# Kernel tuning notes

Hardware: AMD Instinct MI355X
Metric: run time of the kernel (lower is better)

The kernel has to match this reference:

```python
import jax, jax.numpy as jnp
import numpy as np

B, NP, L, C, NA = 16, 512, 20, 3, 50
RATIO = 0.8
K = int(np.ceil(RATIO * NP))  # 410 nodes kept per graph
N = B * NP
E = 6 * N
NF, EF = 13, 4
EPS = 1e-5


def _graph_norm(x, w, b, ms):
    # PyG GraphNorm called WITHOUT batch in the source -> single global graph
    mean = x.mean(0)
    out = x - ms * mean
    var = (out * out).mean(0)
    return w * out / jnp.sqrt(var + EPS) + b


def _forward(x, pan_w, lin1_w, lin1_b, norm1_w, norm1_b, norm1_ms,
             pool_p, pool_beta, gat_wl, gat_bl, gat_wr, gat_br, gat_att, gat_bias,
             norm2_w, norm2_b, norm2_ms,
             val1_w, val1_b, val2_w, val2_b, val3_w, val3_b,
             adv1_w, adv1_b, adv2_w, adv2_b, adv3_w, adv3_b,
             edge_index, current_node_ids, action_mask):
    src, dst = edge_index[0], edge_index[1]
    # PANConv builds SparseTensor(row=edge_index[1], col=edge_index[0]) -> row = target
    A = jnp.zeros((B, NP, NP), x.dtype).at[dst // NP, dst % NP, src % NP].set(1.0)
    eyeB = jnp.broadcast_to(jnp.eye(NP, dtype=x.dtype), A.shape)

    # panentropy: M = sum_{i=0..L} w_i * A^i  (dense per graph)
    def step(carry, wi):
        tmp, acc = carry
        tmp = tmp @ A
        return (tmp, acc + wi * tmp), None
    (_, M), _ = jax.lax.scan(step, (eyeB, pan_w[0] * eyeB), pan_w[1:])
    deg = M.sum(-1)                                   # row sums
    dis = jnp.where(deg > 0, 1.0 / jnp.sqrt(deg), 0.0)
    Mn = dis[:, :, None] * M * dis[:, None, :]        # D^-1/2 M D^-1/2

    # conv1: propagate (Mn @ x) then Linear
    x3 = x.reshape(B, NP, NF)
    h = jnp.einsum('bij,bjf->bif', Mn, x3) @ lin1_w + lin1_b   # [B,NP,C]
    x1 = jax.nn.relu(_graph_norm(h.reshape(N, C), norm1_w, norm1_b, norm1_ms))  # [N,C]
    h = x1.reshape(B, NP, C)

    # PANPooling: score = tanh(b0 * <x,p> + b1 * colsum(Mn)); keep top K per graph
    score = jnp.tanh(pool_beta[0] * (h * pool_p).sum(-1) + pool_beta[1] * Mn.sum(-2))
    vals, idx = jax.lax.top_k(score, K)                        # [B,K]
    xp = jnp.take_along_axis(h, idx[:, :, None], axis=1) * vals[..., None]
    Mg = jax.vmap(lambda m, i: m[i][:, i])(Mn, idx)            # filtered adjacency [B,K,K]
    mask = (jnp.swapaxes(Mg, 1, 2) != 0) | jnp.eye(K, dtype=bool)  # mask[b,i,j]: edge j->i (+self loops)

    # GATv2Conv, heads=1, eval mode (no dropout), edge_attr not passed in source
    xl = xp @ gat_wl + gat_bl
    xr = xp @ gat_wr + gat_br
    e = jax.nn.leaky_relu(xr[:, :, None, :] + xl[:, None, :, :], 0.2)  # [B,i,j,C]
    logits = jnp.where(mask, jnp.einsum('bijc,c->bij', e, gat_att), -1e9)
    alpha = jax.nn.softmax(logits, axis=-1)
    g = jnp.einsum('bij,bjc->bic', alpha, xl) + gat_bias

    g = jax.nn.relu(_graph_norm(g.reshape(B * K, C), norm2_w, norm2_b, norm2_ms)).reshape(B, K, C)
    gp = g.sum(1)                                              # global_add_pool [B,C]

    # source uses POOLED bincount cumsum offsets to index the pre-pool arrays (faithful)
    gidx = current_node_ids + jnp.arange(B, dtype=current_node_ids.dtype) * K
    feat = jnp.concatenate([x[gidx], x1[gidx], gp], axis=1)    # [B,19]

    a = jax.nn.relu(feat @ adv1_w + adv1_b)
    a = jax.nn.relu(a @ adv2_w + adv2_b)
    a = a @ adv3_w + adv3_b
    v = jax.nn.relu(feat @ val1_w + val1_b)
    v = jax.nn.relu(v @ val2_w + val2_b)
    v = v @ val3_w + val3_b
    q = v + (a - a.mean(1, keepdims=True))
    return jnp.where(action_mask == 0, -1e8, q)


def setup_inputs() -> dict:
    key = jax.random.key(0)
    ks = list(jax.random.split(key, 40))
    nk = lambda: ks.pop()
    # within-graph random edges so the PyG-style batch structure is valid
    g = jax.random.randint(nk(), (E,), 0, B)
    u = jax.random.randint(nk(), (E,), 0, NP)
    v = jax.random.randint(nk(), (E,), 0, NP)
    edge_index = jnp.stack([g * NP + u, g * NP + v]).astype(jnp.int32)

    def lin(k, i, o):
        k1, k2 = jax.random.split(k)
        return (jax.random.normal(k1, (i, o), jnp.float32) / np.sqrt(i),
                jax.random.normal(k2, (o,), jnp.float32) * 0.01)

    lin1_w, lin1_b = lin(nk(), NF, C)
    gat_wl, gat_bl = lin(nk(), C, C)
    gat_wr, gat_br = lin(nk(), C, C)
    val1_w, val1_b = lin(nk(), 19, 10)
    val2_w, val2_b = lin(nk(), 10, 5)
    val3_w, val3_b = lin(nk(), 5, 1)
    adv1_w, adv1_b = lin(nk(), 19, 10)
    adv2_w, adv2_b = lin(nk(), 10, 5)
    adv3_w, adv3_b = lin(nk(), 5, NA)
    return dict(
        x=jax.random.normal(nk(), (N, NF), jnp.float32),
        edge_index=edge_index,
        edge_attr=jax.random.normal(nk(), (E, EF), jnp.float32),
        batch=jnp.arange(N, dtype=jnp.int32) // NP,
        current_node_ids=jax.random.randint(nk(), (B,), 0, NP),
        action_mask=jax.random.randint(nk(), (B, NA), 0, 2),
        pan_w=jax.random.uniform(nk(), (L + 1,), jnp.float32) * 0.5,
        lin1_w=lin1_w, lin1_b=lin1_b,
        norm1_w=jnp.ones(C), norm1_b=jnp.zeros(C), norm1_ms=jnp.ones(C),
        pool_p=jax.random.normal(nk(), (C,), jnp.float32),
        pool_beta=jnp.array([0.5, 0.5], jnp.float32),
        gat_wl=gat_wl, gat_bl=gat_bl, gat_wr=gat_wr, gat_br=gat_br,
        gat_att=jax.random.normal(nk(), (C,), jnp.float32),
        gat_bias=jax.random.normal(nk(), (C,), jnp.float32) * 0.01,
        norm2_w=jnp.ones(C), norm2_b=jnp.zeros(C), norm2_ms=jnp.ones(C),
        val1_w=val1_w, val1_b=val1_b, val2_w=val2_w, val2_b=val2_b,
        val3_w=val3_w, val3_b=val3_b,
        adv1_w=adv1_w, adv1_b=adv1_b, adv2_w=adv2_w, adv2_b=adv2_b,
        adv3_w=adv3_w, adv3_b=adv3_b,
    )


def reference(x, edge_index, edge_attr, batch, current_node_ids, action_mask,
              pan_w, lin1_w, lin1_b, norm1_w, norm1_b, norm1_ms,
              pool_p, pool_beta, gat_wl, gat_bl, gat_wr, gat_br, gat_att, gat_bias,
              norm2_w, norm2_b, norm2_ms,
              val1_w, val1_b, val2_w, val2_b, val3_w, val3_b,
              adv1_w, adv1_b, adv2_w, adv2_b, adv3_w, adv3_b):
    del edge_attr, batch  # received by the torch forward but never consumed
    return _forward(x, pan_w, lin1_w, lin1_b, norm1_w, norm1_b, norm1_ms,
                    pool_p, pool_beta, gat_wl, gat_bl, gat_wr, gat_br, gat_att, gat_bias,
                    norm2_w, norm2_b, norm2_ms,
                    val1_w, val1_b, val2_w, val2_b, val3_w, val3_b,
                    adv1_w, adv1_b, adv2_w, adv2_b, adv3_w, adv3_b,
                    edge_index, current_node_ids, action_mask)
```

## Files before the change

kernel.cpp:

```cpp
#include <hip/hip_runtime.h>
#include <hip/hip_bf16.h>
#include <stdint.h>
#include <math.h>

#define BB   16
#define NPn  512
#define LLp  20
#define NAa  50
#define KKk  410
#define NNt  (BB * NPn)
#define EEe  (6 * NNt)
#define NFf  13
#define KPAD 416
#define KP2  448
#define EPSf 1e-5f
#define QCLMP 1e6f
#define MAXD 28
#define PADR 512

__device__ __forceinline__ float r17_sane(float v) {
    if (!(v == v)) return 0.0f;
    return fminf(fmaxf(v, -1e15f), 1e15f);
}

__device__ __forceinline__ int r19_wmaxdeg(const int (&iF)[MAXD]) {
    int deg = 0;
#pragma unroll
    for (int j = 0; j < MAXD; ++j) deg += (iF[j] != PADR) ? 1 : 0;
#pragma unroll
    for (int off = 32; off; off >>= 1) {
        const int o = __shfl_xor(deg, off);
        deg = o > deg ? o : deg;
    }
    return deg;
}

__device__ __forceinline__ float r19_gsum(const float* __restrict__ rp,
                                          const int (&iF)[MAXD], int dm) {
    float s = 0.0f;
    s += rp[iF[0]]; s += rp[iF[1]]; s += rp[iF[2]]; s += rp[iF[3]];
    if (dm > 4) {
        s += rp[iF[4]]; s += rp[iF[5]]; s += rp[iF[6]]; s += rp[iF[7]];
        if (dm > 8) {
            s += rp[iF[8]]; s += rp[iF[9]]; s += rp[iF[10]]; s += rp[iF[11]];
            if (dm > 12) {
                s += rp[iF[12]]; s += rp[iF[13]]; s += rp[iF[14]]; s += rp[iF[15]];
                if (dm > 16) {
                    s += rp[iF[16]]; s += rp[iF[17]]; s += rp[iF[18]]; s += rp[iF[19]];
                    if (dm > 20) {
                        s += rp[iF[20]]; s += rp[iF[21]]; s += rp[iF[22]]; s += rp[iF[23]];
                        if (dm > 24) {
                            s += rp[iF[24]]; s += rp[iF[25]]; s += rp[iF[26]]; s += rp[iF[27]];
                        }
                    }
                }
            }
        }
    }
    return s;
}

__device__ __forceinline__ void r19_gor(const uint2* __restrict__ rp,
                                        const int (&iF)[MAXD], int dm, uint2& r) {
    {
        const uint2 v0 = rp[iF[0]], v1 = rp[iF[1]], v2 = rp[iF[2]], v3 = rp[iF[3]];
        r.x |= v0.x | v1.x | v2.x | v3.x;
        r.y |= v0.y | v1.y | v2.y | v3.y;
    }
    if (dm > 4) {
        const uint2 v0 = rp[iF[4]], v1 = rp[iF[5]], v2 = rp[iF[6]], v3 = rp[iF[7]];
        r.x |= v0.x | v1.x | v2.x | v3.x;
        r.y |= v0.y | v1.y | v2.y | v3.y;
        if (dm > 8) {
            const uint2 w0 = rp[iF[8]], w1 = rp[iF[9]], w2 = rp[iF[10]], w3 = rp[iF[11]];
            r.x |= w0.x | w1.x | w2.x | w3.x;
            r.y |= w0.y | w1.y | w2.y | w3.y;
            if (dm > 12) {
                const uint2 u0 = rp[iF[12]], u1 = rp[iF[13]], u2 = rp[iF[14]], u3 = rp[iF[15]];
                r.x |= u0.x | u1.x | u2.x | u3.x;
                r.y |= u0.y | u1.y | u2.y | u3.y;
                if (dm > 16) {
                    const uint2 a0 = rp[iF[16]], a1 = rp[iF[17]], a2 = rp[iF[18]], a3 = rp[iF[19]];
                    r.x |= a0.x | a1.x | a2.x | a3.x;
                    r.y |= a0.y | a1.y | a2.y | a3.y;
                    if (dm > 20) {
                        const uint2 b0 = rp[iF[20]], b1 = rp[iF[21]], b2 = rp[iF[22]], b3 = rp[iF[23]];
                        r.x |= b0.x | b1.x | b2.x | b3.x;
                        r.y |= b0.y | b1.y | b2.y | b3.y;
                        if (dm > 24) {
                            const uint2 c0 = rp[iF[24]], c1 = rp[iF[25]], c2 = rp[iF[26]], c3 = rp[iF[27]];
                            r.x |= c0.x | c1.x | c2.x | c3.x;
                            r.y |= c0.y | c1.y | c2.y | c3.y;
                        }
                    }
                }
            }
        }
    }
}

__global__ __launch_bounds__(256) void r17_scatter(
    const int* __restrict__ ei,
    uint32_t* __restrict__ fwdb, uint32_t* __restrict__ trsb)
{
    const int e = blockIdx.x * 256 + threadIdx.x;
    if (e < EEe) {
        const int src = ei[e], dst = ei[EEe + e];
        atomicOr(&fwdb[(size_t)dst * 16 + ((src & 511) >> 5)], 1u << (src & 31));
        atomicOr(&trsb[(size_t)src * 16 + ((dst & 511) >> 5)], 1u << (dst & 31));
    }
}

__global__ __launch_bounds__(256) void r17_extract(
    const uint32_t* __restrict__ fwdb, const uint32_t* __restrict__ trsb,
    unsigned short* __restrict__ csrF, unsigned short* __restrict__ csrT)
{
    const int t = blockIdx.x * 256 + threadIdx.x;
    const int node = t & 8191;
    const uint32_t* bs = (t < 8192) ? (fwdb + (size_t)node * 16)
                                    : (trsb + (size_t)node * 16);
    unsigned short* cs = (t < 8192) ? csrF : csrT;
    int cnt = 0;
    for (int w = 0; w < 16; ++w) {
        uint32_t bits = bs[w];
        while (bits) {
            const int u = (w << 5) + __ffs(bits) - 1;
            bits &= bits - 1;
            if (cnt < MAXD) cs[(size_t)cnt * 8192 + node] = (unsigned short)u;
            ++cnt;
        }
    }
    for (int j = cnt; j < MAXD; ++j) cs[(size_t)j * 8192 + node] = PADR;
}

__global__ __launch_bounds__(512) void r19_mid(
    const float* __restrict__ x,
    const unsigned short* __restrict__ csrF,
    const unsigned short* __restrict__ csrT,
    const float* __restrict__ panw,
    const float* __restrict__ l1w, const float* __restrict__ l1b,
    float* __restrict__ h_raw, float* __restrict__ colsum,
    uint32_t* __restrict__ Rb)
{
    __shared__ __align__(16) uint32_t sbuf[2052];
    const int b = blockIdx.x, y = blockIdx.y, t = threadIdx.x;
    const int node = b * 512 + t;

    int iF[MAXD];
#pragma unroll
    for (int j = 0; j < MAXD; ++j) iF[j] = (int)csrF[(size_t)j * 8192 + node];
    const int dmF = r19_wmaxdeg(iF);

    if (y < 4) {
        const int c = y;
        float* pa  = (float*)sbuf;
        float* pb  = (float*)(sbuf + 513);
        float* wsh = (float*)(sbuf + 1026);
        if (t < 21) wsh[t] = panw[t];

        pa[t] = 1.0f;
        if (t == 0) { pa[512] = 0.0f; pb[512] = 0.0f; }
        __syncthreads();
        float dacc = wsh[0];
        {
            float* rp = pa; float* rn = pb;
            for (int i = 1; i <= LLp; ++i) {
                const float s = r19_gsum(rp, iF, dmF);
                rn[t] = s;
                dacc += wsh[i] * s;
                __syncthreads();
                float* tp = rp; rp = rn; rn = tp;
            }
        }
        const float d0 = (dacc > 0.0f) ? 1.0f / sqrtf(dacc) : 0.0f;

        int idx[MAXD];
        int dm2;
        if (c == 3) {
#pragma unroll
            for (int j = 0; j < MAXD; ++j) idx[j] = (int)csrT[(size_t)j * 8192 + node];
            dm2 = r19_wmaxdeg(idx);
        } else {
#pragma unroll
            for (int j = 0; j < MAXD; ++j) idx[j] = iF[j];
            dm2 = dmF;
        }
        float seed;
        if (c < 3) {
            float xw = 0.0f;
            const float* xr = x + (size_t)node * NFf;
            for (int f = 0; f < NFf; ++f) xw += xr[f] * l1w[f * 3 + c];
            seed = d0 * xw;
        } else {
            seed = d0;
        }
        pa[t] = seed;
        if (t == 0) { pa[512] = 0.0f; pb[512] = 0.0f; }
        __syncthreads();
        float acc = wsh[0] * seed;
        {
            float* rp = pa; float* rn = pb;
            for (int i = 1; i <= LLp; ++i) {
                const float s = r19_gsum(rp, idx, dm2);
                rn[t] = s;
                acc += wsh[i] * s;
                __syncthreads();
                float* tp = rp; rp = rn; rn = tp;
            }
        }
        if (c < 3) h_raw[(size_t)node * 3 + c] = r17_sane(d0 * acc + l1b[c]);
        else       colsum[node] = r17_sane(d0 * acc);
    } else {
        const int q = y - 4;
        uint2* R1 = (uint2*)sbuf;
        uint2* R2 = R1 + 513;
        uint2 seed;
        seed.x = ((t >> 5) == 2 * q)     ? (1u << (t & 31)) : 0u;
        seed.y = ((t >> 5) == 2 * q + 1) ? (1u << (t & 31)) : 0u;
        R1[t] = seed;
        if (t == 0) {
            uint2 z; z.x = 0u; z.y = 0u;
            R1[512] = z; R2[512] = z;
        }
        __syncthreads();
        uint2* Rp = R1; uint2* Rn = R2;
        for (int i = 0; i < LLp; ++i) {
            uint2 r = Rp[t];
            r19_gor(Rp, iF, dmF, r);
            Rn[t] = r;
            __syncthreads();
            uint2* tp = Rp; Rp = Rn; Rn = tp;
        }
        *(uint2*)(&Rb[(size_t)node * 16 + 2 * q]) = Rp[t];
    }
}

__global__ __launch_bounds__(512) void r19_pool(
    const float* __restrict__ h_raw,
    const float* __restrict__ colsum,
    const uint32_t* __restrict__ Rb,
    const float* n1w, const float* n1b, const float* n1ms,
    const float* poolp, const float* poolb,
    const float* gwl, const float* gbl,
    float* __restrict__ x1,
    float* __restrict__ xpg,
    float4* __restrict__ xlg,
    int*   __restrict__ kidxg,
    uint32_t* __restrict__ RTg)
{
    __shared__ __align__(16) uint32_t pg[2208];
    float* sc   = (float*)pg;
    float* mv   = (float*)(pg + 512);
    float* wred = (float*)(pg + 520);
    float* xpS  = (float*)(pg + 544);
    int*   kidx = (int*)(pg + 1792);
    const int b = blockIdx.x, t = threadIdx.x;
    const int lane = t & 63, wv = t >> 6;
    const float inv_n = 1.0f / (float)NNt;

    float hv0[16], hv1[16], hv2[16];
    float p0 = 0.0f, p1 = 0.0f, p2 = 0.0f;
#pragma unroll
    for (int k = 0; k < 16; ++k) {
        const float* hr = h_raw + (size_t)(k * 512 + t) * 3;
        hv0[k] = hr[0]; hv1[k] = hr[1]; hv2[k] = hr[2];
        p0 += hv0[k]; p1 += hv1[k]; p2 += hv2[k];
    }
#pragma unroll
    for (int off = 32; off; off >>= 1) {
        p0 += __shfl_xor(p0, off); p1 += __shfl_xor(p1, off); p2 += __shfl_xor(p2, off);
    }
    if (lane == 0) { wred[wv * 3 + 0] = p0; wred[wv * 3 + 1] = p1; wred[wv * 3 + 2] = p2; }
    __syncthreads();
    if (t < 3) {
        float s = 0.0f;
        for (int w = 0; w < 8; ++w) s += wred[w * 3 + t];
        mv[t] = s * inv_n;
    }
    __syncthreads();
    const float mm0 = n1ms[0] * mv[0], mm1 = n1ms[1] * mv[1], mm2 = n1ms[2] * mv[2];
    float q0 = 0.0f, q1 = 0.0f, q2 = 0.0f;
#pragma unroll
    for (int k = 0; k < 16; ++k) {
        const float d0 = hv0[k] - mm0, d1 = hv1[k] - mm1, d2 = hv2[k] - mm2;
        q0 += d0 * d0; q1 += d1 * d1; q2 += d2 * d2;
    }
#pragma unroll
    for (int off = 32; off; off >>= 1) {
        q0 += __shfl_xor(q0, off); q1 += __shfl_xor(q1, off); q2 += __shfl_xor(q2, off);
    }
    if (lane == 0) { wred[wv * 3 + 0] = q0; wred[wv * 3 + 1] = q1; wred[wv * 3 + 2] = q2; }
    __syncthreads();
    if (t < 3) {
        float s = 0.0f;
        for (int w = 0; w < 8; ++w) s += wred[w * 3 + t];
        mv[3 + t] = s * inv_n;
    }
    __syncthreads();

    const float mmv[3] = { mm0, mm1, mm2 };
    float xv[3];
#pragma unroll
    for (int c = 0; c < 3; ++c) {
        const float iv = 1.0f / sqrtf(fmaxf(mv[3 + c], 0.0f) + EPSf);
        const float o  = h_raw[(size_t)(b * NPn + t) * 3 + c] - mmv[c];
        const float tt = n1w[c] * o * iv + n1b[c];
        xv[c] = fmaxf(tt, 0.0f);
        x1[(size_t)(b * NPn + t) * 3 + c] = xv[c];
    }
    float s = poolb[0] * (xv[0] * poolp[0] + xv[1] * poolp[1] + xv[2] * poolp[2])
            + poolb[1] * colsum[b * NPn + t];
    s = tanhf(s);
    if (!(s == s)) s = 0.0f;
    sc[t] = s;
    __syncthreads();

    int cnt = 0;
    for (int u = 0; u < NPn; u += 4) {
        const float4 s4 = *(const float4*)(sc + u);
        cnt += ((s4.x > s) || (s4.x == s && (u + 0) < t)) ? 1 : 0;
        cnt += ((s4.y > s) || (s4.y == s && (u + 1) < t)) ? 1 : 0;
        cnt += ((s4.z > s) || (s4.z == s && (u + 2) < t)) ? 1 : 0;
        cnt += ((s4.w > s) || (s4.w == s && (u + 3) < t)) ? 1 : 0;
    }
    if (cnt < KKk) {
        const float xp0 = xv[0] * s, xp1 = xv[1] * s, xp2 = xv[2] * s;
        kidx[cnt] = t;
        xpS[cnt * 3 + 0] = xp0;
        xpS[cnt * 3 + 1] = xp1;
        xpS[cnt * 3 + 2] = xp2;
        kidxg[b * KPAD + cnt] = t;
        xpg[(size_t)(b * KPAD + cnt) * 3 + 0] = xp0;
        xpg[(size_t)(b * KPAD + cnt) * 3 + 1] = xp1;
        xpg[(size_t)(b * KPAD + cnt) * 3 + 2] = xp2;
    }
    __syncthreads();

    float Wl[9];
#pragma unroll
    for (int i2 = 0; i2 < 9; ++i2) Wl[i2] = gwl[i2];
    const float Bl0 = gbl[0], Bl1 = gbl[1], Bl2 = gbl[2];
    if (t < KP2) {
        float xl0, xl1, xl2;
        uint32_t* RT = RTg + (size_t)b * 16 * KP2 + t;
        if (t < KKk) {
            const float c0 = xpS[t * 3 + 0];
            const float c1 = xpS[t * 3 + 1];
            const float c2 = xpS[t * 3 + 2];
            xl0 = c0 * Wl[0] + c1 * Wl[3] + c2 * Wl[6] + Bl0;
            xl1 = c0 * Wl[1] + c1 * Wl[4] + c2 * Wl[7] + Bl1;
            xl2 = c0 * Wl[2] + c1 * Wl[5] + c2 * Wl[8] + Bl2;
            const uint4* rr = (const uint4*)(Rb + (size_t)(b * NPn + kidx[t]) * 16);
            const uint4 r0 = rr[0], r1 = rr[1], r2 = rr[2], r3 = rr[3];
            RT[ 0 * KP2] = r0.x; RT[ 1 * KP2] = r0.y; RT[ 2 * KP2] = r0.z; RT[ 3 * KP2] = r0.w;
            RT[ 4 * KP2] = r1.x; RT[ 5 * KP2] = r1.y; RT[ 6 * KP2] = r1.z; RT[ 7 * KP2] = r1.w;
            RT[ 8 * KP2] = r2.x; RT[ 9 * KP2] = r2.y; RT[10 * KP2] = r2.z; RT[11 * KP2] = r2.w;
            RT[12 * KP2] = r3.x; RT[13 * KP2] = r3.y; RT[14 * KP2] = r3.z; RT[15 * KP2] = r3.w;
        } else {
            xl0 = 0.0f; xl1 = 0.0f; xl2 = 0.0f;
#pragma unroll
            for (int w = 0; w < 16; ++w) RT[w * KP2] = 0u;
        }
        xlg[(size_t)(b * KP2 + t)] = make_float4(xl0, xl1, xl2, 0.0f);
    }
}

__global__ __launch_bounds__(512) void r19_gat(
    const float* __restrict__ xpg,
    const float4* __restrict__ xlg,
    const int* __restrict__ kidxg,
    const uint32_t* __restrict__ RTg,
    const float* __restrict__ gwr, const float* __restrict__ gbr,
    const float* __restrict__ gatt, const float* __restrict__ gbias,
    float* __restrict__ g_raw)
{
    const int b = blockIdx.x, y = blockIdx.y, t = threadIdx.x;
    const int lane = t & 63, wv = t >> 6;
    const int i = y * 8 + wv;
    if (i >= KKk) return;

    float Wr[9];
#pragma unroll
    for (int k = 0; k < 9; ++k) Wr[k] = gwr[k];
    const float Br0 = gbr[0], Br1 = gbr[1], Br2 = gbr[2];
    const float At0 = gatt[0], At1 = gatt[1], At2 = gatt[2];
    const float Gb0 = gbias[0], Gb1 = gbias[1], Gb2 = gbias[2];

    const int bi = kidxg[b * KPAD + i];
    const float c0 = xpg[(size_t)(b * KPAD + i) * 3 + 0];
    const float c1 = xpg[(size_t)(b * KPAD + i) * 3 + 1];
    const float c2 = xpg[(size_t)(b * KPAD + i) * 3 + 2];
    const float xr0 = c0 * Wr[0] + c1 * Wr[3] + c2 * Wr[6] + Br0;
    const float xr1 = c0 * Wr[1] + c1 * Wr[4] + c2 * Wr[7] + Br1;
    const float xr2 = c0 * Wr[2] + c1 * Wr[5] + c2 * Wr[8] + Br2;

    const uint32_t mbit = 1u << (bi & 31);
    const uint32_t* Rw = RTg + (size_t)(b * 16 + (bi >> 5)) * KP2;
    const float4* xlb = xlg + (size_t)b * KP2;

    float mx = -3e38f, lsum = 0.0f, b0 = 0.0f, b1 = 0.0f, b2 = 0.0f;
#pragma unroll
    for (int it = 0; it < 7; ++it) {
        const int j = lane + it * 64;
        const uint32_t rw = Rw[j];
        const float4 xlv = xlb[j];
        const float xl0 = xlv.x, xl1 = xlv.y, xl2 = xlv.z;
        const bool valid = (rw & mbit) || (j == i);
        float e0 = xr0 + xl0; e0 = e0 > 0.0f ? e0 : 0.2f * e0;
        float e1 = xr1 + xl1; e1 = e1 > 0.0f ? e1 : 0.2f * e1;
        float e2 = xr2 + xl2; e2 = e2 > 0.0f ? e2 : 0.2f * e2;
        const float sv = At0 * e0 + At1 * e1 + At2 * e2;
        if (valid) {
            if (sv > mx) {
                const float r = __expf(mx - sv);
                lsum *= r; b0 *= r; b1 *= r; b2 *= r;
                mx = sv;
            }
            const float pj = __expf(sv - mx);
            lsum += pj;
            b0 += pj * xl0; b1 += pj * xl1; b2 += pj * xl2;
        }
    }
#pragma unroll
    for (int off = 32; off; off >>= 1) {
        const float mo = __shfl_xor(mx, off);
        const float lo = __shfl_xor(lsum, off);
        const float d0 = __shfl_xor(b0, off);
        const float d1 = __shfl_xor(b1, off);
        const float d2 = __shfl_xor(b2, off);
        const float M  = fmaxf(mx, mo);
        const float ea = __expf(mx - M), eb = __expf(mo - M);
        lsum = lsum * ea + lo * eb;
        b0 = b0 * ea + d0 * eb;
        b1 = b1 * ea + d1 * eb;
        b2 = b2 * ea + d2 * eb;
        mx = M;
    }
    if (lane == 0) {
        const float rl = 1.0f / fmaxf(lsum, 1e-30f);
        g_raw[(size_t)(b * KPAD + i) * 3 + 0] = r17_sane(b0 * rl + Gb0);
        g_raw[(size_t)(b * KPAD + i) * 3 + 1] = r17_sane(b1 * rl + Gb1);
        g_raw[(size_t)(b * KPAD + i) * 3 + 2] = r17_sane(b2 * rl + Gb2);
    }
}

__global__ __launch_bounds__(512) void r17_head(
    const float* __restrict__ g_raw,
    const float* __restrict__ x1,
    const float* __restrict__ x,
    const int* __restrict__ cnid,
    const int* __restrict__ amask,
    const float* n2w, const float* n2b, const float* n2ms,
    const float* v1w, const float* v1b,
    const float* v2w, const float* v2b,
    const float* v3w, const float* v3b,
    const float* a1w, const float* a1b,
    const float* a2w, const float* a2b,
    const float* a3w, const float* a3b,
    float* __restrict__ out)
{
    __shared__ float wred[24];
    __shared__ float mv[6];
    __shared__ float gp[3];
    __shared__ float feat[19];
    __shared__ float h1a[10], h1v[10], h2a[5], h2v[5];
    __shared__ float a3[50];
    __shared__ float vout_s, amean_s;
    const int b = blockIdx.x, t = threadIdx.x;
    const int lane = t & 63, wv = t >> 6;
    const float denom = 1.0f / (float)(BB * KKk);

    float gv0[13], gv1[13], gv2[13];
    float p0 = 0.0f, p1 = 0.0f, p2 = 0.0f;
#pragma unroll
    for (int k = 0; k < 13; ++k) {
        const int r = k * 512 + t;
        float q0 = 0.0f, q1 = 0.0f, q2 = 0.0f;
        if (r < BB * KKk) {
            const int bq = r / KKk, iq = r - bq * KKk;
            const float* gr = g_raw + (size_t)(bq * KPAD + iq) * 3;
            q0 = gr[0]; q1 = gr[1]; q2 = gr[2];
        }
        gv0[k] = q0; gv1[k] = q1; gv2[k] = q2;
        p0 += q0; p1 += q1; p2 += q2;
    }
#pragma unroll
    for (int off = 32; off; off >>= 1) {
        p0 += __shfl_xor(p0, off); p1 += __shfl_xor(p1, off); p2 += __shfl_xor(p2, off);
    }
    if (lane == 0) { wred[wv * 3 + 0] = p0; wred[wv * 3 + 1] = p1; wred[wv * 3 + 2] = p2; }
    __syncthreads();
    if (t < 3) {
        float s = 0.0f;
        for (int w = 0; w < 8; ++w) s += wred[w * 3 + t];
        mv[t] = s * denom;
    }
    __syncthreads();
    const float mm0 = n2ms[0] * mv[0], mm1 = n2ms[1] * mv[1], mm2 = n2ms[2] * mv[2];
    float q0a = 0.0f, q1a = 0.0f, q2a = 0.0f;
#pragma unroll
    for (int k = 0; k < 13; ++k) {
        const int r = k * 512 + t;
        if (r < BB * KKk) {
            const float d0 = gv0[k] - mm0, d1 = gv1[k] - mm1, d2 = gv2[k] - mm2;
            q0a += d0 * d0; q1a += d1 * d1; q2a += d2 * d2;
        }
    }
#pragma unroll
    for (int off = 32; off; off >>= 1) {
        q0a += __shfl_xor(q0a, off); q1a += __shfl_xor(q1a, off); q2a += __shfl_xor(q2a, off);
    }
    if (lane == 0) { wred[wv * 3 + 0] = q0a; wred[wv * 3 + 1] = q1a; wred[wv * 3 + 2] = q2a; }
    __syncthreads();
    if (t < 3) {
        float s = 0.0f;
        for (int w = 0; w < 8; ++w) s += wred[w * 3 + t];
        mv[3 + t] = s * denom;
    }
    __syncthreads();

    const float mmv[3] = { mm0, mm1, mm2 };
    float s3[3] = { 0.0f, 0.0f, 0.0f };
    if (t < KKk) {
        const size_t r = (size_t)(b * KPAD + t) * 3;
#pragma unroll
        for (int c = 0; c < 3; ++c) {
            const float iv = 1.0f / sqrtf(fmaxf(mv[3 + c], 0.0f) + EPSf);
            s3[c] = fmaxf((g_raw[r + c] - mmv[c]) * iv * n2w[c] + n2b[c], 0.0f);
        }
    }
    float g0 = s3[0], g1 = s3[1], g2 = s3[2];
#pragma unroll
    for (int off = 32; off; off >>= 1) {
        g0 += __shfl_xor(g0, off); g1 += __shfl_xor(g1, off); g2 += __shfl_xor(g2, off);
    }
    if (lane == 0) { wred[wv * 3 + 0] = g0; wred[wv * 3 + 1] = g1; wred[wv * 3 + 2] = g2; }
    __syncthreads();
    if (t < 3) {
        float s = 0.0f;
        for (int w = 0; w < 8; ++w) s += wred[w * 3 + t];
        gp[t] = s;
    }
    __syncthreads();

    if (t < 19) {
        const int gidx = cnid[b] + b * KKk;
        float fv;
        if (t < 13)      fv = x[(size_t)gidx * NFf + t];
        else if (t < 16) fv = x1[(size_t)gidx * 3 + (t - 13)];
        else             fv = gp[t - 16];
        feat[t] = fv;
    }
    __syncthreads();

    if (t < 10) {
        float s = a1b[t];
        for (int f = 0; f < 19; ++f) s += feat[f] * a1w[f * 10 + t];
        h1a[t] = fmaxf(s, 0.0f);
    } else if (t >= 64 && t < 74) {
        const int j = t - 64;
        float s = v1b[j];
        for (int f = 0; f < 19; ++f) s += feat[f] * v1w[f * 10 + j];
        h1v[j] = fmaxf(s, 0.0f);
    }
    __syncthreads();
    if (t < 5) {
        float s = a2b[t];
        for (int k = 0; k < 10; ++k) s += h1a[k] * a2w[k * 5 + t];
        h2a[t] = fmaxf(s, 0.0f);
    } else if (t >= 64 && t < 69) {
        const int j = t - 64;
        float s = v2b[j];
        for (int k = 0; k < 10; ++k) s += h1v[k] * v2w[k * 5 + j];
        h2v[j] = fmaxf(s, 0.0f);
    }
    __syncthreads();
    if (t < 50) {
        float s = a3b[t];
        for (int k = 0; k < 5; ++k) s += h2a[k] * a3w[k * 50 + t];
        a3[t] = s;
    } else if (t == 64) {
        float s = v3b[0];
        for (int k = 0; k < 5; ++k) s += h2v[k] * v3w[k];
        vout_s = s;
    }
    __syncthreads();
    if (t == 0) {
        float s = 0.0f;
        for (int k = 0; k < 50; ++k) s += a3[k];
        amean_s = s * (1.0f / 50.0f);
    }
    __syncthreads();
    if (t < 50) {
        float q = vout_s + a3[t] - amean_s;
        if (!(q == q)) q = 0.0f;
        q = fminf(fmaxf(q, -QCLMP), QCLMP);
        out[b * NAa + t] = (amask[b * NAa + t] == 0) ? -1e8f : q;
    }
}

extern "C" void kernel_launch(void* const* d_in, const int* in_sizes, int n_in,
                              void* d_out, int out_size, void* d_ws, size_t ws_size,
                              hipStream_t stream) {
    (void)in_sizes; (void)n_in; (void)out_size;
    const float* x     = (const float*)d_in[0];
    const int* ei      = (const int*)d_in[1];
    const int* cnid    = (const int*)d_in[4];
    const int* amask   = (const int*)d_in[5];
    const float* panw  = (const float*)d_in[6];
    const float* l1w   = (const float*)d_in[7];
    const float* l1b   = (const float*)d_in[8];
    const float* n1w   = (const float*)d_in[9];
    const float* n1b   = (const float*)d_in[10];
    const float* n1ms  = (const float*)d_in[11];
    const float* poolp = (const float*)d_in[12];
    const float* poolb = (const float*)d_in[13];
    const float* gwl   = (const float*)d_in[14];
    const float* gbl   = (const float*)d_in[15];
    const float* gwr   = (const float*)d_in[16];
    const float* gbr   = (const float*)d_in[17];
    const float* gatt  = (const float*)d_in[18];
    const float* gbias = (const float*)d_in[19];
    const float* n2w   = (const float*)d_in[20];
    const float* n2b   = (const float*)d_in[21];
    const float* n2ms  = (const float*)d_in[22];
    const float* v1w   = (const float*)d_in[23];
    const float* v1b   = (const float*)d_in[24];
    const float* v2w   = (const float*)d_in[25];
    const float* v2b   = (const float*)d_in[26];
    const float* v3w   = (const float*)d_in[27];
    const float* v3b   = (const float*)d_in[28];
    const float* a1w   = (const float*)d_in[29];
    const float* a1b   = (const float*)d_in[30];
    const float* a2w   = (const float*)d_in[31];
    const float* a2b   = (const float*)d_in[32];
    const float* a3w   = (const float*)d_in[33];
    const float* a3b   = (const float*)d_in[34];
    float* out         = (float*)d_out;

    uint8_t* wsb = (uint8_t*)d_ws;
    uint32_t* fwdb = (uint32_t*)wsb;
    uint32_t* trsb = (uint32_t*)(wsb + 524288);
    uint32_t* Rb   = (uint32_t*)(wsb + 1048576);
    unsigned short* csrF = (unsigned short*)(wsb + 1572864);
    unsigned short* csrT = csrF + (size_t)MAXD * 8192;
    float* h_raw  = (float*)(csrT + (size_t)MAXD * 8192);
    float* x1     = h_raw + (size_t)NNt * 3;
    float* colsum = x1 + (size_t)NNt * 3;
    float* g_raw  = colsum + NNt;
    float* xpg    = g_raw + (size_t)BB * KPAD * 3;
    float4* xlg   = (float4*)(xpg + (size_t)BB * KPAD * 3);
    int*   kidxg  = (int*)(xlg + (size_t)BB * KP2);
    uint32_t* RTg = (uint32_t*)(kidxg + (size_t)BB * KPAD);
    const size_t needed = 1572864
                        + 2 * (size_t)MAXD * 8192 * 2
                        + ((size_t)(2 * NNt * 3 + NNt
                           + 2 * BB * KPAD * 3)) * 4
                        + (size_t)BB * KP2 * 16
                        + (size_t)BB * KPAD * 4
                        + (size_t)BB * 16 * KP2 * 4;
    if (ws_size < needed) return;

    hipMemsetAsync(fwdb, 0, 1048576, stream);
    r17_scatter<<<dim3((EEe + 255) / 256), dim3(256), 0, stream>>>(ei, fwdb, trsb);
    r17_extract<<<dim3(64), dim3(256), 0, stream>>>(fwdb, trsb, csrF, csrT);
    r19_mid<<<dim3(16, 12), dim3(512), 0, stream>>>(x, csrF, csrT, panw, l1w, l1b,
                                                    h_raw, colsum, Rb);
    r19_pool<<<dim3(16), dim3(512), 0, stream>>>(h_raw, colsum, Rb,
                                                 n1w, n1b, n1ms, poolp, poolb,
                                                 gwl, gbl,
                                                 x1, xpg, xlg, kidxg, RTg);
    r19_gat<<<dim3(16, 52), dim3(512), 0, stream>>>(xpg, xlg, kidxg, RTg,
                                                    gwr, gbr, gatt, gbias, g_raw);
    r17_head<<<dim3(16), dim3(512), 0, stream>>>(g_raw, x1, x, cnid, amask,
                                                 n2w, n2b, n2ms, v1w, v1b, v2w, v2b, v3w, v3b,
                                                 a1w, a1b, a2w, a2b, a3w, a3b, out);
}
```

Baseline: 201.6 us.

## Fuse all stages into one persistent kernel with software grid barriers

Replaces the memset plus six separate kernel launches with a single 192-block persistent kernel. Stages are separated by atomic-counter grid barriers, and only a small barrier memset remains. The aim is to remove per-launch overhead and the inter-kernel gaps in a latency-bound pipeline. The trade-offs are spin-wait barrier cost, the assumption that all 192 blocks are co-resident, and reduced parallelism in stages that previously used more blocks (for example the GAT stage's 16x52 grid).

```diff
diff --git a/kernel.cpp b/kernel.cpp
--- a/kernel.cpp
+++ b/kernel.cpp
@@ -1,5 +1,4 @@
 #include <hip/hip_runtime.h>
-#include <hip/hip_bf16.h>
 #include <stdint.h>
 #include <math.h>
 
@@ -17,10 +16,26 @@
 #define QCLMP 1e6f
 #define MAXD 28
 #define PADR 512
+#define NBLK 192
+#define NWAVE (NBLK * 8)
 
 __device__ __forceinline__ float r17_sane(float v) {
     if (!(v == v)) return 0.0f;
     return fminf(fmaxf(v, -1e15f), 1e15f);
+}
+
+__device__ __forceinline__ void r20_gridbar(uint32_t* bar) {
+    __syncthreads();
+    if (threadIdx.x == 0) {
+        __threadfence();
+        __hip_atomic_fetch_add(bar, 1u, __ATOMIC_ACQ_REL, __HIP_MEMORY_SCOPE_AGENT);
+        while (__hip_atomic_load(bar, __ATOMIC_ACQUIRE, __HIP_MEMORY_SCOPE_AGENT)
+               < (uint32_t)NBLK) {
+            __builtin_amdgcn_s_sleep(2);
+        }
+        __threadfence();
+    }
+    __syncthreads();
 }
 
 __device__ __forceinline__ int r19_wmaxdeg(const int (&iF)[MAXD]) {
@@ -99,503 +114,486 @@
     }
 }
 
-__global__ __launch_bounds__(256) void r17_scatter(
-    const int* __restrict__ ei,
-    uint32_t* __restrict__ fwdb, uint32_t* __restrict__ trsb)
+struct R20P {
+    const float* x; const int* ei; const int* cnid; const int* amask;
+    const float* panw; const float* l1w; const float* l1b;
+    const float* n1w; const float* n1b; const float* n1ms;
+    const float* poolp; const float* poolb;
+    const float* gwl; const float* gbl; const float* gwr; const float* gbr;
+    const float* gatt; const float* gbias;
+    const float* n2w; const float* n2b; const float* n2ms;
+    const float* v1w; const float* v1b; const float* v2w; const float* v2b;
+    const float* v3w; const float* v3b;
+    const float* a1w; const float* a1b; const float* a2w; const float* a2b;
+    const float* a3w; const float* a3b;
+    uint32_t* fwdb; uint32_t* trsb; uint32_t* bar; uint32_t* Rb;
+    unsigned short* csrF; unsigned short* csrT;
+    float* h_raw; float* x1; float* colsum; float* g_raw;
+    float* xpg; float4* xlg; int* kidxg; uint32_t* RTg;
+    float* out;
+};
+
+__global__ __launch_bounds__(512) void r20_mega(R20P p)
 {
-    const int e = blockIdx.x * 256 + threadIdx.x;
-    if (e < EEe) {
-        const int src = ei[e], dst = ei[EEe + e];
-        atomicOr(&fwdb[(size_t)dst * 16 + ((src & 511) >> 5)], 1u << (src & 31));
-        atomicOr(&trsb[(size_t)src * 16 + ((dst & 511) >> 5)], 1u << (dst & 31));
-    }
-}
-
-__global__ __launch_bounds__(256) void r17_extract(
-    const uint32_t* __restrict__ fwdb, const uint32_t* __restrict__ trsb,
-    unsigned short* __restrict__ csrF, unsigned short* __restrict__ csrT)
-{
-    const int t = blockIdx.x * 256 + threadIdx.x;
-    const int node = t & 8191;
-    const uint32_t* bs = (t < 8192) ? (fwdb + (size_t)node * 16)
-                                    : (trsb + (size_t)node * 16);
-    unsigned short* cs = (t < 8192) ? csrF : csrT;
-    int cnt = 0;
-    for (int w = 0; w < 16; ++w) {
-        uint32_t bits = bs[w];
-        while (bits) {
-            const int u = (w << 5) + __ffs(bits) - 1;
-            bits &= bits - 1;
-            if (cnt < MAXD) cs[(size_t)cnt * 8192 + node] = (unsigned short)u;
-            ++cnt;
-        }
-    }
-    for (int j = cnt; j < MAXD; ++j) cs[(size_t)j * 8192 + node] = PADR;
-}
-
-__global__ __launch_bounds__(512) void r19_mid(
-    const float* __restrict__ x,
-    const unsigned short* __restrict__ csrF,
-    const unsigned short* __restrict__ csrT,
-    const float* __restrict__ panw,
-    const float* __restrict__ l1w, const float* __restrict__ l1b,
-    float* __restrict__ h_raw, float* __restrict__ colsum,
-    uint32_t* __restrict__ Rb)
-{
-    __shared__ __align__(16) uint32_t sbuf[2052];
-    const int b = blockIdx.x, y = blockIdx.y, t = threadIdx.x;
-    const int node = b * 512 + t;
-
-    int iF[MAXD];
-#pragma unroll
-    for (int j = 0; j < MAXD; ++j) iF[j] = (int)csrF[(size_t)j * 8192 + node];
-    const int dmF = r19_wmaxdeg(iF);
-
-    if (y < 4) {
-        const int c = y;
-        float* pa  = (float*)sbuf;
-        float* pb  = (float*)(sbuf + 513);
-        float* wsh = (float*)(sbuf + 1026);
-        if (t < 21) wsh[t] = panw[t];
-
-        pa[t] = 1.0f;
-        if (t == 0) { pa[512] = 0.0f; pb[512] = 0.0f; }
-        __syncthreads();
-        float dacc = wsh[0];
-        {
-            float* rp = pa; float* rn = pb;
-            for (int i = 1; i <= LLp; ++i) {
-                const float s = r19_gsum(rp, iF, dmF);
-                rn[t] = s;
-                dacc += wsh[i] * s;
+    __shared__ __align__(16) uint32_t sbuf[2208];
+    const int blk = blockIdx.x, t = threadIdx.x;
+    const int gtid = blk * 512 + t;
+    const int lane = t & 63, wv = t >> 6;
+
+    if (gtid < 65536) ((uint4*)p.fwdb)[gtid] = make_uint4(0u, 0u, 0u, 0u);
+    r20_gridbar(p.bar + 0);
+
+    if (gtid < EEe) {
+        const int src = p.ei[gtid], dst = p.ei[EEe + gtid];
+        atomicOr(&p.fwdb[(size_t)dst * 16 + ((src & 511) >> 5)], 1u << (src & 31));
+        atomicOr(&p.trsb[(size_t)src * 16 + ((dst & 511) >> 5)], 1u << (dst & 31));
+    }
+    r20_gridbar(p.bar + 1);
+
+    if (gtid < 16384) {
+        const int node = gtid & 8191;
+        const uint32_t* bs = (gtid < 8192) ? (p.fwdb + (size_t)node * 16)
+                                           : (p.trsb + (size_t)node * 16);
+        unsigned short* cs = (gtid < 8192) ? p.csrF : p.csrT;
+        int cnt = 0;
+        for (int w = 0; w < 16; ++w) {
+            uint32_t bits = bs[w];
+            while (bits) {
+                const int u = (w << 5) + __ffs(bits) - 1;
+                bits &= bits - 1;
+                if (cnt < MAXD) cs[(size_t)cnt * 8192 + node] = (unsigned short)u;
+                ++cnt;
+            }
+        }
+        for (int j = cnt; j < MAXD; ++j) cs[(size_t)j * 8192 + node] = PADR;
+    }
+    r20_gridbar(p.bar + 2);
+
+    {
+        const int b = blk / 12, y = blk % 12;
+        const int node = b * 512 + t;
+        int iF[MAXD];
+#pragma unroll
+        for (int j = 0; j < MAXD; ++j) iF[j] = (int)p.csrF[(size_t)j * 8192 + node];
+        const int dmF = r19_wmaxdeg(iF);
+
+        if (y < 4) {
+            const int c = y;
+            float* pa  = (float*)sbuf;
+            float* pb  = (float*)(sbuf + 513);
+            float* wsh = (float*)(sbuf + 1026);
+            if (t < 21) wsh[t] = p.panw[t];
+
+            pa[t] = 1.0f;
+            if (t == 0) { pa[512] = 0.0f; pb[512] = 0.0f; }
+            __syncthreads();
+            float dacc = wsh[0];
+            {
+                float* rp = pa; float* rn = pb;
+                for (int i = 1; i <= LLp; ++i) {
+                    const float s = r19_gsum(rp, iF, dmF);
+                    rn[t] = s;
+                    dacc += wsh[i] * s;
+                    __syncthreads();
+                    float* tp = rp; rp = rn; rn = tp;
+                }
+            }
+            const float d0 = (dacc > 0.0f) ? 1.0f / sqrtf(dacc) : 0.0f;
+
+            int idx[MAXD];
+            int dm2;
+            if (c == 3) {
+#pragma unroll
+                for (int j = 0; j < MAXD; ++j) idx[j] = (int)p.csrT[(size_t)j * 8192 + node];
+                dm2 = r19_wmaxdeg(idx);
+            } else {
+#pragma unroll
+                for (int j = 0; j < MAXD; ++j) idx[j] = iF[j];
+                dm2 = dmF;
+            }
+            float seed;
+            if (c < 3) {
+                float xw = 0.0f;
+                const float* xr = p.x + (size_t)node * NFf;
+                for (int f = 0; f < NFf; ++f) xw += xr[f] * p.l1w[f * 3 + c];
+                seed = d0 * xw;
+            } else {
+                seed = d0;
+            }
+            pa[t] = seed;
+            if (t == 0) { pa[512] = 0.0f; pb[512] = 0.0f; }
+            __syncthreads();
+            float acc = wsh[0] * seed;
+            {
+                float* rp = pa; float* rn = pb;
+                for (int i = 1; i <= LLp; ++i) {
+                    const float s = r19_gsum(rp, idx, dm2);
+                    rn[t] = s;
+                    acc += wsh[i] * s;
+                    __syncthreads();
+                    float* tp = rp; rp = rn; rn = tp;
+                }
+            }
+            if (c < 3) p.h_raw[(size_t)node * 3 + c] = r17_sane(d0 * acc + p.l1b[c]);
+            else       p.colsum[node] = r17_sane(d0 * acc);
+        } else {
+            const int q = y - 4;
+            uint2* R1 = (uint2*)sbuf;
+            uint2* R2 = R1 + 513;
+            uint2 seed;
+            seed.x = ((t >> 5) == 2 * q)     ? (1u << (t & 31)) : 0u;
+            seed.y = ((t >> 5) == 2 * q + 1) ? (1u << (t & 31)) : 0u;
+            R1[t] = seed;
+            if (t == 0) {
+                uint2 z; z.x = 0u; z.y = 0u;
+                R1[512] = z; R2[512] = z;
+            }
+            __syncthreads();
+            uint2* Rp = R1; uint2* Rn = R2;
+            for (int i = 0; i < LLp; ++i) {
+                uint2 r = Rp[t];
+                r19_gor(Rp, iF, dmF, r);
+                Rn[t] = r;
                 __syncthreads();
-                float* tp = rp; rp = rn; rn = tp;
-            }
-        }
-        const float d0 = (dacc > 0.0f) ? 1.0f / sqrtf(dacc) : 0.0f;
-
-        int idx[MAXD];
-        int dm2;
-        if (c == 3) {
-#pragma unroll
-            for (int j = 0; j < MAXD; ++j) idx[j] = (int)csrT[(size_t)j * 8192 + node];
-            dm2 = r19_wmaxdeg(idx);
-        } else {
-#pragma unroll
-            for (int j = 0; j < MAXD; ++j) idx[j] = iF[j];
-            dm2 = dmF;
-        }
-        float seed;
-        if (c < 3) {
-            float xw = 0.0f;
-            const float* xr = x + (size_t)node * NFf;
-            for (int f = 0; f < NFf; ++f) xw += xr[f] * l1w[f * 3 + c];
-            seed = d0 * xw;
-        } else {
-            seed = d0;
-        }
-        pa[t] = seed;
-        if (t == 0) { pa[512] = 0.0f; pb[512] = 0.0f; }
-        __syncthreads();
-        float acc = wsh[0] * seed;
-        {
-            float* rp = pa; float* rn = pb;
-            for (int i = 1; i <= LLp; ++i) {
-                const float s = r19_gsum(rp, idx, dm2);
-                rn[t] = s;
-                acc += wsh[i] * s;
-                __syncthreads();
-                float* tp = rp; rp = rn; rn = tp;
-            }
-        }
-        if (c < 3) h_raw[(size_t)node * 3 + c] = r17_sane(d0 * acc + l1b[c]);
-        else       colsum[node] = r17_sane(d0 * acc);
-    } else {
-        const int q = y - 4;
-        uint2* R1 = (uint2*)sbuf;
-        uint2* R2 = R1 + 513;
-        uint2 seed;
-        seed.x = ((t >> 5) == 2 * q)     ? (1u << (t & 31)) : 0u;
-        seed.y = ((t >> 5) == 2 * q + 1) ? (1u << (t & 31)) : 0u;
-        R1[t] = seed;
-        if (t == 0) {
-            uint2 z; z.x = 0u; z.y = 0u;
-            R1[512] = z; R2[512] = z;
-        }
-        __syncthreads();
-        uint2* Rp = R1; uint2* Rn = R2;
-        for (int i = 0; i < LLp; ++i) {
-            uint2 r = Rp[t];
-            r19_gor(Rp, iF, dmF, r);
-            Rn[t] = r;
-            __syncthreads();
-            uint2* tp = Rp; Rp = Rn; Rn = tp;
-        }
-        *(uint2*)(&Rb[(size_t)node * 16 + 2 * q]) = Rp[t];
-    }
-}
-
-__global__ __launch_bounds__(512) void r19_pool(
-    const float* __restrict__ h_raw,
-    const float* __restrict__ colsum,
-    const uint32_t* __restrict__ Rb,
-    const float* n1w, const float* n1b, const float* n1ms,
-    const float* poolp, const float* poolb,
-    const float* gwl, const float* gbl,
-    float* __restrict__ x1,
-    float* __restrict__ xpg,
-    float4* __restrict__ xlg,
-    int*   __restrict__ kidxg,
-    uint32_t* __restrict__ RTg)
-{
-    __shared__ __align__(16) uint32_t pg[2208];
-    float* sc   = (float*)pg;
-    float* mv   = (float*)(pg + 512);
-    float* wred = (float*)(pg + 520);
-    float* xpS  = (float*)(pg + 544);
-    int*   kidx = (int*)(pg + 1792);
-    const int b = blockIdx.x, t = threadIdx.x;
-    const int lane = t & 63, wv = t >> 6;
-    const float inv_n = 1.0f / (float)NNt;
-
-    float hv0[16], hv1[16], hv2[16];
-    float p0 = 0.0f, p1 = 0.0f, p2 = 0.0f;
-#pragma unroll
-    for (int k = 0; k < 16; ++k) {
-        const float* hr = h_raw + (size_t)(k * 512 + t) * 3;
-        hv0[k] = hr[0]; hv1[k] = hr[1]; hv2[k] = hr[2];
-        p0 += hv0[k]; p1 += hv1[k]; p2 += hv2[k];
-    }
-#pragma unroll
-    for (int off = 32; off; off >>= 1) {
-        p0 += __shfl_xor(p0, off); p1 += __shfl_xor(p1, off); p2 += __shfl_xor(p2, off);
-    }
-    if (lane == 0) { wred[wv * 3 + 0] = p0; wred[wv * 3 + 1] = p1; wred[wv * 3 + 2] = p2; }
-    __syncthreads();
-    if (t < 3) {
-        float s = 0.0f;
-        for (int w = 0; w < 8; ++w) s += wred[w * 3 + t];
-        mv[t] = s * inv_n;
-    }
-    __syncthreads();
-    const float mm0 = n1ms[0] * mv[0], mm1 = n1ms[1] * mv[1], mm2 = n1ms[2] * mv[2];
-    float q0 = 0.0f, q1 = 0.0f, q2 = 0.0f;
-#pragma unroll
-    for (int k = 0; k < 16; ++k) {
-        const float d0 = hv0[k] - mm0, d1 = hv1[k] - mm1, d2 = hv2[k] - mm2;
-        q0 += d0 * d0; q1 += d1 * d1; q2 += d2 * d2;
-    }
-#pragma unroll
-    for (int off = 32; off; off >>= 1) {
-        q0 += __shfl_xor(q0, off); q1 += __shfl_xor(q1, off); q2 += __shfl_xor(q2, off);
-    }
-    if (lane == 0) { wred[wv * 3 + 0] = q0; wred[wv * 3 + 1] = q1; wred[wv * 3 + 2] = q2; }
-    __syncthreads();
-    if (t < 3) {
-        float s = 0.0f;
-        for (int w = 0; w < 8; ++w) s += wred[w * 3 + t];
-        mv[3 + t] = s * inv_n;
-    }
-    __syncthreads();
-
-    const float mmv[3] = { mm0, mm1, mm2 };
-    float xv[3];
-#pragma unroll
-    for (int c = 0; c < 3; ++c) {
-        const float iv = 1.0f / sqrtf(fmaxf(mv[3 + c], 0.0f) + EPSf);
-        const float o  = h_raw[(size_t)(b * NPn + t) * 3 + c] - mmv[c];
-        const float tt = n1w[c] * o * iv + n1b[c];
-        xv[c] = fmaxf(tt, 0.0f);
-        x1[(size_t)(b * NPn + t) * 3 + c] = xv[c];
-    }
-    float s = poolb[0] * (xv[0] * poolp[0] + xv[1] * poolp[1] + xv[2] * poolp[2])
-            + poolb[1] * colsum[b * NPn + t];
-    s = tanhf(s);
-    if (!(s == s)) s = 0.0f;
-    sc[t] = s;
-    __syncthreads();
-
-    int cnt = 0;
-    for (int u = 0; u < NPn; u += 4) {
-        const float4 s4 = *(const float4*)(sc + u);
-        cnt += ((s4.x > s) || (s4.x == s && (u + 0) < t)) ? 1 : 0;
-        cnt += ((s4.y > s) || (s4.y == s && (u + 1) < t)) ? 1 : 0;
-        cnt += ((s4.z > s) || (s4.z == s && (u + 2) < t)) ? 1 : 0;
-        cnt += ((s4.w > s) || (s4.w == s && (u + 3) < t)) ? 1 : 0;
-    }
-    if (cnt < KKk) {
-        const float xp0 = xv[0] * s, xp1 = xv[1] * s, xp2 = xv[2] * s;
-        kidx[cnt] = t;
-        xpS[cnt * 3 + 0] = xp0;
-        xpS[cnt * 3 + 1] = xp1;
-        xpS[cnt * 3 + 2] = xp2;
-        kidxg[b * KPAD + cnt] = t;
-        xpg[(size_t)(b * KPAD + cnt) * 3 + 0] = xp0;
-        xpg[(size_t)(b * KPAD + cnt) * 3 + 1] = xp1;
-        xpg[(size_t)(b * KPAD + cnt) * 3 + 2] = xp2;
-    }
-    __syncthreads();
-
-    float Wl[9];
-#pragma unroll
-    for (int i2 = 0; i2 < 9; ++i2) Wl[i2] = gwl[i2];
-    const float Bl0 = gbl[0], Bl1 = gbl[1], Bl2 = gbl[2];
-    if (t < KP2) {
-        float xl0, xl1, xl2;
-        uint32_t* RT = RTg + (size_t)b * 16 * KP2 + t;
-        if (t < KKk) {
-            const float c0 = xpS[t * 3 + 0];
-            const float c1 = xpS[t * 3 + 1];
-            const float c2 = xpS[t * 3 + 2];
-            xl0 = c0 * Wl[0] + c1 * Wl[3] + c2 * Wl[6] + Bl0;
-            xl1 = c0 * Wl[1] + c1 * Wl[4] + c2 * Wl[7] + Bl1;
-            xl2 = c0 * Wl[2] + c1 * Wl[5] + c2 * Wl[8] + Bl2;
-            const uint4* rr = (const uint4*)(Rb + (size_t)(b * NPn + kidx[t]) * 16);
-            const uint4 r0 = rr[0], r1 = rr[1], r2 = rr[2], r3 = rr[3];
-            RT[ 0 * KP2] = r0.x; RT[ 1 * KP2] = r0.y; RT[ 2 * KP2] = r0.z; RT[ 3 * KP2] = r0.w;
-            RT[ 4 * KP2] = r1.x; RT[ 5 * KP2] = r1.y; RT[ 6 * KP2] = r1.z; RT[ 7 * KP2] = r1.w;
-            RT[ 8 * KP2] = r2.x; RT[ 9 * KP2] = r2.y; RT[10 * KP2] = r2.z; RT[11 * KP2] = r2.w;
-            RT[12 * KP2] = r3.x; RT[13 * KP2] = r3.y; RT[14 * KP2] = r3.z; RT[15 * KP2] = r3.w;
-        } else {
-            xl0 = 0.0f; xl1 = 0.0f; xl2 = 0.0f;
-#pragma unroll
-            for (int w = 0; w < 16; ++w) RT[w * KP2] = 0u;
-        }
-        xlg[(size_t)(b * KP2 + t)] = make_float4(xl0, xl1, xl2, 0.0f);
-    }
-}
-
-__global__ __launch_bounds__(512) void r19_gat(
-    const float* __restrict__ xpg,
-    const float4* __restrict__ xlg,
-    const int* __restrict__ kidxg,
-    const uint32_t* __restrict__ RTg,
-    const float* __restrict__ gwr, const float* __restrict__ gbr,
-    const float* __restrict__ gatt, const float* __restrict__ gbias,
-    float* __restrict__ g_raw)
-{
-    const int b = blockIdx.x, y = blockIdx.y, t = threadIdx.x;
-    const int lane = t & 63, wv = t >> 6;
-    const int i = y * 8 + wv;
-    if (i >= KKk) return;
-
-    float Wr[9];
-#pragma unroll
-    for (int k = 0; k < 9; ++k) Wr[k] = gwr[k];
-    const float Br0 = gbr[0], Br1 = gbr[1], Br2 = gbr[2];
-    const float At0 = gatt[0], At1 = gatt[1], At2 = gatt[2];
-    const float Gb0 = gbias[0], Gb1 = gbias[1], Gb2 = gbias[2];
-
-    const int bi = kidxg[b * KPAD + i];
-    const float c0 = xpg[(size_t)(b * KPAD + i) * 3 + 0];
-    const float c1 = xpg[(size_t)(b * KPAD + i) * 3 + 1];
-    const float c2 = xpg[(size_t)(b * KPAD + i) * 3 + 2];
-    const float xr0 = c0 * Wr[0] + c1 * Wr[3] + c2 * Wr[6] + Br0;
-    const float xr1 = c0 * Wr[1] + c1 * Wr[4] + c2 * Wr[7] + Br1;
-    const float xr2 = c0 * Wr[2] + c1 * Wr[5] + c2 * Wr[8] + Br2;
-
-    const uint32_t mbit = 1u << (bi & 31);
-    const uint32_t* Rw = RTg + (size_t)(b * 16 + (bi >> 5)) * KP2;
-    const float4* xlb = xlg + (size_t)b * KP2;
-
-    float mx = -3e38f, lsum = 0.0f, b0 = 0.0f, b1 = 0.0f, b2 = 0.0f;
-#pragma unroll
-    for (int it = 0; it < 7; ++it) {
-        const int j = lane + it * 64;
-        const uint32_t rw = Rw[j];
-        const float4 xlv = xlb[j];
-        const float xl0 = xlv.x, xl1 = xlv.y, xl2 = xlv.z;
-        const bool valid = (rw & mbit) || (j == i);
-        float e0 = xr0 + xl0; e0 = e0 > 0.0f ? e0 : 0.2f * e0;
-        float e1 = xr1 + xl1; e1 = e1 > 0.0f ? e1 : 0.2f * e1;
-        float e2 = xr2 + xl2; e2 = e2 > 0.0f ? e2 : 0.2f * e2;
-        const float sv = At0 * e0 + At1 * e1 + At2 * e2;
-        if (valid) {
-            if (sv > mx) {
-                const float r = __expf(mx - sv);
-                lsum *= r; b0 *= r; b1 *= r; b2 *= r;
-                mx = sv;
-            }
-            const float pj = __expf(sv - mx);
-            lsum += pj;
-            b0 += pj * xl0; b1 += pj * xl1; b2 += pj * xl2;
-        }
-    }
-#pragma unroll
-    for (int off = 32; off; off >>= 1) {
-        const float mo = __shfl_xor(mx, off);
-        const float lo = __shfl_xor(lsum, off);
-        const float d0 = __shfl_xor(b0, off);
-        const float d1 = __shfl_xor(b1, off);
-        const float d2 = __shfl_xor(b2, off);
-        const float M  = fmaxf(mx, mo);
-        const float ea = __expf(mx - M), eb = __expf(mo - M);
-        lsum = lsum * ea + lo * eb;
-        b0 = b0 * ea + d0 * eb;
-        b1 = b1 * ea + d1 * eb;
-        b2 = b2 * ea + d2 * eb;
-        mx = M;
-    }
-    if (lane == 0) {
-        const float rl = 1.0f / fmaxf(lsum, 1e-30f);
-        g_raw[(size_t)(b * KPAD + i) * 3 + 0] = r17_sane(b0 * rl + Gb0);
-        g_raw[(size_t)(b * KPAD + i) * 3 + 1] = r17_sane(b1 * rl + Gb1);
-        g_raw[(size_t)(b * KPAD + i) * 3 + 2] = r17_sane(b2 * rl + Gb2);
-    }
-}
-
-__global__ __launch_bounds__(512) void r17_head(
-    const float* __restrict__ g_raw,
-    const float* __restrict__ x1,
-    const float* __restrict__ x,
-    const int* __restrict__ cnid,
-    const int* __restrict__ amask,
-    const float* n2w, const float* n2b, const float* n2ms,
-    const float* v1w, const float* v1b,
-    const float* v2w, const float* v2b,
-    const float* v3w, const float* v3b,
-    const float* a1w, const float* a1b,
-    const float* a2w, const float* a2b,
-    const float* a3w, const float* a3b,
-    float* __restrict__ out)
-{
-    __shared__ float wred[24];
-    __shared__ float mv[6];
-    __shared__ float gp[3];
-    __shared__ float feat[19];
-    __shared__ float h1a[10], h1v[10], h2a[5], h2v[5];
-    __shared__ float a3[50];
-    __shared__ float vout_s, amean_s;
-    const int b = blockIdx.x, t = threadIdx.x;
-    const int lane = t & 63, wv = t >> 6;
-    const float denom = 1.0f / (float)(BB * KKk);
-
-    float gv0[13], gv1[13], gv2[13];
-    float p0 = 0.0f, p1 = 0.0f, p2 = 0.0f;
-#pragma unroll
-    for (int k = 0; k < 13; ++k) {
-        const int r = k * 512 + t;
+                uint2* tp = Rp; Rp = Rn; Rn = tp;
+            }
+            *(uint2*)(&p.Rb[(size_t)node * 16 + 2 * q]) = Rp[t];
+        }
+    }
+    r20_gridbar(p.bar + 3);
+
+    if (blk < BB) {
+        const int b = blk;
+        float* sc   = (float*)sbuf;
+        float* mv   = (float*)(sbuf + 512);
+        float* wred = (float*)(sbuf + 520);
+        float* xpS  = (float*)(sbuf + 544);
+        int*   kidx = (int*)(sbuf + 1792);
+        const float inv_n = 1.0f / (float)NNt;
+
+        float hv0[16], hv1[16], hv2[16];
+        float p0 = 0.0f, p1 = 0.0f, p2 = 0.0f;
+#pragma unroll
+        for (int k = 0; k < 16; ++k) {
+            const float* hr = p.h_raw + (size_t)(k * 512 + t) * 3;
+            hv0[k] = hr[0]; hv1[k] = hr[1]; hv2[k] = hr[2];
+            p0 += hv0[k]; p1 += hv1[k]; p2 += hv2[k];
+        }
+#pragma unroll
+        for (int off = 32; off; off >>= 1) {
+            p0 += __shfl_xor(p0, off); p1 += __shfl_xor(p1, off); p2 += __shfl_xor(p2, off);
+        }
+        if (lane == 0) { wred[wv * 3 + 0] = p0; wred[wv * 3 + 1] = p1; wred[wv * 3 + 2] = p2; }
+        __syncthreads();
+        if (t < 3) {
+            float s = 0.0f;
+            for (int w = 0; w < 8; ++w) s += wred[w * 3 + t];
+            mv[t] = s * inv_n;
+        }
+        __syncthreads();
+        const float mm0 = p.n1ms[0] * mv[0], mm1 = p.n1ms[1] * mv[1], mm2 = p.n1ms[2] * mv[2];
         float q0 = 0.0f, q1 = 0.0f, q2 = 0.0f;
-        if (r < BB * KKk) {
-            const int bq = r / KKk, iq = r - bq * KKk;
-            const float* gr = g_raw + (size_t)(bq * KPAD + iq) * 3;
-            q0 = gr[0]; q1 = gr[1]; q2 = gr[2];
-        }
-        gv0[k] = q0; gv1[k] = q1; gv2[k] = q2;
-        p0 += q0; p1 += q1; p2 += q2;
-    }
-#pragma unroll
-    for (int off = 32; off; off >>= 1) {
-        p0 += __shfl_xor(p0, off); p1 += __shfl_xor(p1, off); p2 += __shfl_xor(p2, off);
-    }
-    if (lane == 0) { wred[wv * 3 + 0] = p0; wred[wv * 3 + 1] = p1; wred[wv * 3 + 2] = p2; }
-    __syncthreads();
-    if (t < 3) {
-        float s = 0.0f;
-        for (int w = 0; w < 8; ++w) s += wred[w * 3 + t];
-        mv[t] = s * denom;
-    }
-    __syncthreads();
-    const float mm0 = n2ms[0] * mv[0], mm1 = n2ms[1] * mv[1], mm2 = n2ms[2] * mv[2];
-    float q0a = 0.0f, q1a = 0.0f, q2a = 0.0f;
-#pragma unroll
-    for (int k = 0; k < 13; ++k) {
-        const int r = k * 512 + t;
-        if (r < BB * KKk) {
-            const float d0 = gv0[k] - mm0, d1 = gv1[k] - mm1, d2 = gv2[k] - mm2;
-            q0a += d0 * d0; q1a += d1 * d1; q2a += d2 * d2;
-        }
-    }
-#pragma unroll
-    for (int off = 32; off; off >>= 1) {
-        q0a += __shfl_xor(q0a, off); q1a += __shfl_xor(q1a, off); q2a += __shfl_xor(q2a, off);
-    }
-    if (lane == 0) { wred[wv * 3 + 0] = q0a; wred[wv * 3 + 1] = q1a; wred[wv * 3 + 2] = q2a; }
-    __syncthreads();
-    if (t < 3) {
-        float s = 0.0f;
-        for (int w = 0; w < 8; ++w) s += wred[w * 3 + t];
-        mv[3 + t] = s * denom;
-    }
-    __syncthreads();
-
-    const float mmv[3] = { mm0, mm1, mm2 };
-    float s3[3] = { 0.0f, 0.0f, 0.0f };
-    if (t < KKk) {
-        const size_t r = (size_t)(b * KPAD + t) * 3;
+#pragma unroll
+        for (int k = 0; k < 16; ++k) {
+            const float d0 = hv0[k] - mm0, d1 = hv1[k] - mm1, d2 = hv2[k] - mm2;
+            q0 += d0 * d0; q1 += d1 * d1; q2 += d2 * d2;
+        }
+#pragma unroll
+        for (int off = 32; off; off >>= 1) {
+            q0 += __shfl_xor(q0, off); q1 += __shfl_xor(q1, off); q2 += __shfl_xor(q2, off);
+        }
+        if (lane == 0) { wred[wv * 3 + 0] = q0; wred[wv * 3 + 1] = q1; wred[wv * 3 + 2] = q2; }
+        __syncthreads();
+        if (t < 3) {
+            float s = 0.0f;
+            for (int w = 0; w < 8; ++w) s += wred[w * 3 + t];
+            mv[3 + t] = s * inv_n;
+        }
+        __syncthreads();
+
+        const float mmv[3] = { mm0, mm1, mm2 };
+        float xv[3];
 #pragma unroll
         for (int c = 0; c < 3; ++c) {
             const float iv = 1.0f / sqrtf(fmaxf(mv[3 + c], 0.0f) + EPSf);
-            s3[c] = fmaxf((g_raw[r + c] - mmv[c]) * iv * n2w[c] + n2b[c], 0.0f);
-        }
-    }
-    float g0 = s3[0], g1 = s3[1], g2 = s3[2];
-#pragma unroll
-    for (int off = 32; off; off >>= 1) {
-        g0 += __shfl_xor(g0, off); g1 += __shfl_xor(g1, off); g2 += __shfl_xor(g2, off);
-    }
-    if (lane == 0) { wred[wv * 3 + 0] = g0; wred[wv * 3 + 1] = g1; wred[wv * 3 + 2] = g2; }
-    __syncthreads();
-    if (t < 3) {
-        float s = 0.0f;
-        for (int w = 0; w < 8; ++w) s += wred[w * 3 + t];
-        gp[t] = s;
-    }
-    __syncthreads();
-
-    if (t < 19) {
-        const int gidx = cnid[b] + b * KKk;
-        float fv;
-        if (t < 13)      fv = x[(size_t)gidx * NFf + t];
-        else if (t < 16) fv = x1[(size_t)gidx * 3 + (t - 13)];
-        else             fv = gp[t - 16];
-        feat[t] = fv;
-    }
-    __syncthreads();
-
-    if (t < 10) {
-        float s = a1b[t];
-        for (int f = 0; f < 19; ++f) s += feat[f] * a1w[f * 10 + t];
-        h1a[t] = fmaxf(s, 0.0f);
-    } else if (t >= 64 && t < 74) {
-        const int j = t - 64;
-        float s = v1b[j];
-        for (int f = 0; f < 19; ++f) s += feat[f] * v1w[f * 10 + j];
-        h1v[j] = fmaxf(s, 0.0f);
-    }
-    __syncthreads();
-    if (t < 5) {
-        float s = a2b[t];
-        for (int k = 0; k < 10; ++k) s += h1a[k] * a2w[k * 5 + t];
-        h2a[t] = fmaxf(s, 0.0f);
-    } else if (t >= 64 && t < 69) {
-        const int j = t - 64;
-        float s = v2b[j];
-        for (int k = 0; k < 10; ++k) s += h1v[k] * v2w[k * 5 + j];
-        h2v[j] = fmaxf(s, 0.0f);
-    }
-    __syncthreads();
-    if (t < 50) {
-        float s = a3b[t];
-        for (int k = 0; k < 5; ++k) s += h2a[k] * a3w[k * 50 + t];
-        a3[t] = s;
-    } else if (t == 64) {
-        float s = v3b[0];
-        for (int k = 0; k < 5; ++k) s += h2v[k] * v3w[k];
-        vout_s = s;
-    }
-    __syncthreads();
-    if (t == 0) {
-        float s = 0.0f;
-        for (int k = 0; k < 50; ++k) s += a3[k];
-        amean_s = s * (1.0f / 50.0f);
-    }
-    __syncthreads();
-    if (t < 50) {
-        float q = vout_s + a3[t] - amean_s;
-        if (!(q == q)) q = 0.0f;
-        q = fminf(fmaxf(q, -QCLMP), QCLMP);
-        out[b * NAa + t] = (amask[b * NAa + t] == 0) ? -1e8f : q;
+            const float o  = p.h_raw[(size_t)(b * NPn + t) * 3 + c] - mmv[c];
+            const float tt = p.n1w[c] * o * iv + p.n1b[c];
+            xv[c] = fmaxf(tt, 0.0f);
+            p.x1[(size_t)(b * NPn + t) * 3 + c] = xv[c];
+        }
+        float s = p.poolb[0] * (xv[0] * p.poolp[0] + xv[1] * p.poolp[1] + xv[2] * p.poolp[2])
+                + p.poolb[1] * p.colsum[b * NPn + t];
+        s = tanhf(s);
+        if (!(s == s)) s = 0.0f;
+        sc[t] = s;
+        __syncthreads();
+
+        int cnt = 0;
+        for (int u = 0; u < NPn; u += 4) {
+            const float4 s4 = *(const float4*)(sc + u);
+            cnt += ((s4.x > s) || (s4.x == s && (u + 0) < t)) ? 1 : 0;
+            cnt += ((s4.y > s) || (s4.y == s && (u + 1) < t)) ? 1 : 0;
+            cnt += ((s4.z > s) || (s4.z == s && (u + 2) < t)) ? 1 : 0;
+            cnt += ((s4.w > s) || (s4.w == s && (u + 3) < t)) ? 1 : 0;
+        }
+        if (cnt < KKk) {
+            const float xp0 = xv[0] * s, xp1 = xv[1] * s, xp2 = xv[2] * s;
+            kidx[cnt] = t;
+            xpS[cnt * 3 + 0] = xp0;
+            xpS[cnt * 3 + 1] = xp1;
+            xpS[cnt * 3 + 2] = xp2;
+            p.kidxg[b * KPAD + cnt] = t;
+            p.xpg[(size_t)(b * KPAD + cnt) * 3 + 0] = xp0;
+            p.xpg[(size_t)(b * KPAD + cnt) * 3 + 1] = xp1;
+            p.xpg[(size_t)(b * KPAD + cnt) * 3 + 2] = xp2;
+        }
+        __syncthreads();
+
+        float Wl[9];
+#pragma unroll
+        for (int i2 = 0; i2 < 9; ++i2) Wl[i2] = p.gwl[i2];
+        const float Bl0 = p.gbl[0], Bl1 = p.gbl[1], Bl2 = p.gbl[2];
+        if (t < KP2) {
+            float xl0, xl1, xl2;
+            uint32_t* RT = p.RTg + (size_t)b * 16 * KP2 + t;
+            if (t < KKk) {
+                const float c0 = xpS[t * 3 + 0];
+                const float c1 = xpS[t * 3 + 1];
+                const float c2 = xpS[t * 3 + 2];
+                xl0 = c0 * Wl[0] + c1 * Wl[3] + c2 * Wl[6] + Bl0;
+                xl1 = c0 * Wl[1] + c1 * Wl[4] + c2 * Wl[7] + Bl1;
+                xl2 = c0 * Wl[2] + c1 * Wl[5] + c2 * Wl[8] + Bl2;
+                const uint4* rr = (const uint4*)(p.Rb + (size_t)(b * NPn + kidx[t]) * 16);
+                const uint4 r0 = rr[0], r1 = rr[1], r2 = rr[2], r3 = rr[3];
+                RT[ 0 * KP2] = r0.x; RT[ 1 * KP2] = r0.y; RT[ 2 * KP2] = r0.z; RT[ 3 * KP2] = r0.w;
+                RT[ 4 * KP2] = r1.x; RT[ 5 * KP2] = r1.y; RT[ 6 * KP2] = r1.z; RT[ 7 * KP2] = r1.w;
+                RT[ 8 * KP2] = r2.x; RT[ 9 * KP2] = r2.y; RT[10 * KP2] = r2.z; RT[11 * KP2] = r2.w;
+                RT[12 * KP2] = r3.x; RT[13 * KP2] = r3.y; RT[14 * KP2] = r3.z; RT[15 * KP2] = r3.w;
+            } else {
+                xl0 = 0.0f; xl1 = 0.0f; xl2 = 0.0f;
+#pragma unroll
+                for (int w = 0; w < 16; ++w) RT[w * KP2] = 0u;
+            }
+            p.xlg[(size_t)(b * KP2 + t)] = make_float4(xl0, xl1, xl2, 0.0f);
+        }
+    }
+    r20_gridbar(p.bar + 4);
+
+    {
+        const int wvg = blk * 8 + wv;
+        float Wr[9];
+#pragma unroll
+        for (int k = 0; k < 9; ++k) Wr[k] = p.gwr[k];
+        const float Br0 = p.gbr[0], Br1 = p.gbr[1], Br2 = p.gbr[2];
+        const float At0 = p.gatt[0], At1 = p.gatt[1], At2 = p.gatt[2];
+        const float Gb0 = p.gbias[0], Gb1 = p.gbias[1], Gb2 = p.gbias[2];
+
+        for (int r = wvg; r < BB * KPAD; r += NWAVE) {
+            const int b = r / KPAD, i = r - b * KPAD;
+            if (i >= KKk) continue;
+            const int bi = p.kidxg[b * KPAD + i];
+            const float c0 = p.xpg[(size_t)(b * KPAD + i) * 3 + 0];
+            const float c1 = p.xpg[(size_t)(b * KPAD + i) * 3 + 1];
+            const float c2 = p.xpg[(size_t)(b * KPAD + i) * 3 + 2];
+            const float xr0 = c0 * Wr[0] + c1 * Wr[3] + c2 * Wr[6] + Br0;
+            const float xr1 = c0 * Wr[1] + c1 * Wr[4] + c2 * Wr[7] + Br1;
+            const float xr2 = c0 * Wr[2] + c1 * Wr[5] + c2 * Wr[8] + Br2;
+
+            const uint32_t mbit = 1u << (bi & 31);
+            const uint32_t* Rw = p.RTg + (size_t)(b * 16 + (bi >> 5)) * KP2;
+            const float4* xlb = p.xlg + (size_t)b * KP2;
+
+            float mx = -3e38f, lsum = 0.0f, b0 = 0.0f, b1 = 0.0f, b2 = 0.0f;
+#pragma unroll
+            for (int it = 0; it < 7; ++it) {
+                const int j = lane + it * 64;
+                const uint32_t rw = Rw[j];
+                const float4 xlv = xlb[j];
+                const float xl0 = xlv.x, xl1 = xlv.y, xl2 = xlv.z;
+                const bool valid = (rw & mbit) || (j == i);
+                float e0 = xr0 + xl0; e0 = e0 > 0.0f ? e0 : 0.2f * e0;
+                float e1 = xr1 + xl1; e1 = e1 > 0.0f ? e1 : 0.2f * e1;
+                float e2 = xr2 + xl2; e2 = e2 > 0.0f ? e2 : 0.2f * e2;
+                const float sv = At0 * e0 + At1 * e1 + At2 * e2;
+                if (valid) {
+                    if (sv > mx) {
+                        const float rr = __expf(mx - sv);
+                        lsum *= rr; b0 *= rr; b1 *= rr; b2 *= rr;
+                        mx = sv;
+                    }
+                    const float pj = __expf(sv - mx);
+                    lsum += pj;
+                    b0 += pj * xl0; b1 += pj * xl1; b2 += pj * xl2;
+                }
+            }
+#pragma unroll
+            for (int off = 32; off; off >>= 1) {
+                const float mo = __shfl_xor(mx, off);
+                const float lo = __shfl_xor(lsum, off);
+                const float d0 = __shfl_xor(b0, off);
+                const float d1 = __shfl_xor(b1, off);
+                const float d2 = __shfl_xor(b2, off);
+                const float M  = fmaxf(mx, mo);
+                const float ea = __expf(mx - M), eb = __expf(mo - M);
+                lsum = lsum * ea + lo * eb;
+                b0 = b0 * ea + d0 * eb;
+                b1 = b1 * ea + d1 * eb;
+                b2 = b2 * ea + d2 * eb;
+                mx = M;
+            }
+            if (lane == 0) {
+                const float rl = 1.0f / fmaxf(lsum, 1e-30f);
+                p.g_raw[(size_t)(b * KPAD + i) * 3 + 0] = r17_sane(b0 * rl + Gb0);
+                p.g_raw[(size_t)(b * KPAD + i) * 3 + 1] = r17_sane(b1 * rl + Gb1);
+                p.g_raw[(size_t)(b * KPAD + i) * 3 + 2] = r17_sane(b2 * rl + Gb2);
+            }
+        }
+    }
+    r20_gridbar(p.bar + 5);
+
+    if (blk < BB) {
+        const int b = blk;
+        float* sm     = (float*)sbuf;
+        float* wred   = sm;
+        float* mv     = sm + 24;
+        float* gp     = sm + 30;
+        float* feat   = sm + 33;
+        float* h1a    = sm + 52;
+        float* h1v    = sm + 62;
+        float* h2a    = sm + 72;
+        float* h2v    = sm + 77;
+        float* a3     = sm + 82;
+        float* vout_s = sm + 132;
+        float* amean_s= sm + 133;
+        const float denom = 1.0f / (float)(BB * KKk);
+
+        float gv0[13], gv1[13], gv2[13];
+        float p0 = 0.0f, p1 = 0.0f, p2 = 0.0f;
+#pragma unroll
+        for (int k = 0; k < 13; ++k) {
+            const int r = k * 512 + t;
+            float q0 = 0.0f, q1 = 0.0f, q2 = 0.0f;
+            if (r < BB * KKk) {
+                const int bq = r / KKk, iq = r - bq * KKk;
+                const float* gr = p.g_raw + (size_t)(bq * KPAD + iq) * 3;
+                q0 = gr[0]; q1 = gr[1]; q2 = gr[2];
+            }
+            gv0[k] = q0; gv1[k] = q1; gv2[k] = q2;
+            p0 += q0; p1 += q1; p2 += q2;
+        }
+#pragma unroll
+        for (int off = 32; off; off >>= 1) {
+            p0 += __shfl_xor(p0, off); p1 += __shfl_xor(p1, off); p2 += __shfl_xor(p2, off);
+        }
+        if (lane == 0) { wred[wv * 3 + 0] = p0; wred[wv * 3 + 1] = p1; wred[wv * 3 + 2] = p2; }
+        __syncthreads();
+        if (t < 3) {
+            float s = 0.0f;
+            for (int w = 0; w < 8; ++w) s += wred[w * 3 + t];
+            mv[t] = s * denom;
+        }
+        __syncthreads();
+        const float mm0 = p.n2ms[0] * mv[0], mm1 = p.n2ms[1] * mv[1], mm2 = p.n2ms[2] * mv[2];
+        float q0a = 0.0f, q1a = 0.0f, q2a = 0.0f;
+#pragma unroll
+        for (int k = 0; k < 13; ++k) {
+            const int r = k * 512 + t;
+            if (r < BB * KKk) {
+                const float d0 = gv0[k] - mm0, d1 = gv1[k] - mm1, d2 = gv2[k] - mm2;
+                q0a += d0 * d0; q1a += d1 * d1; q2a += d2 * d2;
+            }
+        }
+#pragma unroll
+        for (int off = 32; off; off >>= 1) {
+            q0a += __shfl_xor(q0a, off); q1a += __shfl_xor(q1a, off); q2a += __shfl_xor(q2a, off);
+        }
+        if (lane == 0) { wred[wv * 3 + 0] = q0a; wred[wv * 3 + 1] = q1a; wred[wv * 3 + 2] = q2a; }
+        __syncthreads();
+        if (t < 3) {
+            float s = 0.0f;
+            for (int w = 0; w < 8; ++w) s += wred[w * 3 + t];
+            mv[3 + t] = s * denom;
+        }
+        __syncthreads();
+
+        const float mmv[3] = { mm0, mm1, mm2 };
+        float s3[3] = { 0.0f, 0.0f, 0.0f };
+        if (t < KKk) {
+            const size_t r = (size_t)(b * KPAD + t) * 3;
+#pragma unroll
+            for (int c = 0; c < 3; ++c) {
+                const float iv = 1.0f / sqrtf(fmaxf(mv[3 + c], 0.0f) + EPSf);
+                s3[c] = fmaxf((p.g_raw[r + c] - mmv[c]) * iv * p.n2w[c] + p.n2b[c], 0.0f);
+            }
+        }
+        float g0 = s3[0], g1 = s3[1], g2 = s3[2];
+#pragma unroll
+        for (int off = 32; off; off >>= 1) {
+            g0 += __shfl_xor(g0, off); g1 += __shfl_xor(g1, off); g2 += __shfl_xor(g2, off);
+        }
+        if (lane == 0) { wred[wv * 3 + 0] = g0; wred[wv * 3 + 1] = g1; wred[wv * 3 + 2] = g2; }
+        __syncthreads();
+        if (t < 3) {
+            float s = 0.0f;
+            for (int w = 0; w < 8; ++w) s += wred[w * 3 + t];
+            gp[t] = s;
+        }
+        __syncthreads();
+
+        if (t < 19) {
+            const int gidx = p.cnid[b] + b * KKk;
+            float fv;
+            if (t < 13)      fv = p.x[(size_t)gidx * NFf + t];
+            else if (t < 16) fv = p.x1[(size_t)gidx * 3 + (t - 13)];
+            else             fv = gp[t - 16];
+            feat[t] = fv;
+        }
+        __syncthreads();
+
+        if (t < 10) {
+            float s = p.a1b[t];
+            for (int f = 0; f < 19; ++f) s += feat[f] * p.a1w[f * 10 + t];
+            h1a[t] = fmaxf(s, 0.0f);
+        } else if (t >= 64 && t < 74) {
+            const int j = t - 64;
+            float s = p.v1b[j];
+            for (int f = 0; f < 19; ++f) s += feat[f] * p.v1w[f * 10 + j];
+            h1v[j] = fmaxf(s, 0.0f);
+        }
+        __syncthreads();
+        if (t < 5) {
+            float s = p.a2b[t];
+            for (int k = 0; k < 10; ++k) s += h1a[k] * p.a2w[k * 5 + t];
+            h2a[t] = fmaxf(s, 0.0f);
+        } else if (t >= 64 && t < 69) {
+            const int j = t - 64;
+            float s = p.v2b[j];
+            for (int k = 0; k < 10; ++k) s += h1v[k] * p.v2w[k * 5 + j];
+            h2v[j] = fmaxf(s, 0.0f);
+        }
+        __syncthreads();
+        if (t < 50) {
+            float s = p.a3b[t];
+            for (int k = 0; k < 5; ++k) s += h2a[k] * p.a3w[k * 50 + t];
+            a3[t] = s;
+        } else if (t == 64) {
+            float s = p.v3b[0];
+            for (int k = 0; k < 5; ++k) s += h2v[k] * p.v3w[k];
+            *vout_s = s;
+        }
+        __syncthreads();
+        if (t == 0) {
+            float s = 0.0f;
+            for (int k = 0; k < 50; ++k) s += a3[k];
+            *amean_s = s * (1.0f / 50.0f);
+        }
+        __syncthreads();
+        if (t < 50) {
+            float q = *vout_s + a3[t] - *amean_s;
+            if (!(q == q)) q = 0.0f;
+            q = fminf(fmaxf(q, -QCLMP), QCLMP);
+            p.out[b * NAa + t] = (p.amask[b * NAa + t] == 0) ? -1e8f : q;
+        }
     }
 }
 
@@ -603,76 +601,60 @@
                               void* d_out, int out_size, void* d_ws, size_t ws_size,
                               hipStream_t stream) {
     (void)in_sizes; (void)n_in; (void)out_size;
-    const float* x     = (const float*)d_in[0];
-    const int* ei      = (const int*)d_in[1];
-    const int* cnid    = (const int*)d_in[4];
-    const int* amask   = (const int*)d_in[5];
-    const float* panw  = (const float*)d_in[6];
-    const float* l1w   = (const float*)d_in[7];
-    const float* l1b   = (const float*)d_in[8];
-    const float* n1w   = (const float*)d_in[9];
-    const float* n1b   = (const float*)d_in[10];
-    const float* n1ms  = (const float*)d_in[11];
-    const float* poolp = (const float*)d_in[12];
-    const float* poolb = (const float*)d_in[13];
-    const float* gwl   = (const float*)d_in[14];
-    const float* gbl   = (const float*)d_in[15];
-    const float* gwr   = (const float*)d_in[16];
-    const float* gbr   = (const float*)d_in[17];
-    const float* gatt  = (const float*)d_in[18];
-    const float* gbias = (const float*)d_in[19];
-    const float* n2w   = (const float*)d_in[20];
-    const float* n2b   = (const float*)d_in[21];
-    const float* n2ms  = (const float*)d_in[22];
-    const float* v1w   = (const float*)d_in[23];
-    const float* v1b   = (const float*)d_in[24];
-    const float* v2w   = (const float*)d_in[25];
-    const float* v2b   = (const float*)d_in[26];
-    const float* v3w   = (const float*)d_in[27];
-    const float* v3b   = (const float*)d_in[28];
-    const float* a1w   = (const float*)d_in[29];
-    const float* a1b   = (const float*)d_in[30];
-    const float* a2w   = (const float*)d_in[31];
-    const float* a2b   = (const float*)d_in[32];
-    const float* a3w   = (const float*)d_in[33];
-    const float* a3b   = (const float*)d_in[34];
-    float* out         = (float*)d_out;
+    R20P p;
+    p.x     = (const float*)d_in[0];
+    p.ei    = (const int*)d_in[1];
+    p.cnid  = (const int*)d_in[4];
+    p.amask = (const int*)d_in[5];
+    p.panw  = (const float*)d_in[6];
+    p.l1w   = (const float*)d_in[7];
+    p.l1b   = (const float*)d_in[8];
+    p.n1w   = (const float*)d_in[9];
+    p.n1b   = (const float*)d_in[10];
+    p.n1ms  = (const float*)d_in[11];
+    p.poolp = (const float*)d_in[12];
+    p.poolb = (const float*)d_in[13];
+    p.gwl   = (const float*)d_in[14];
+    p.gbl   = (const float*)d_in[15];
+    p.gwr   = (const float*)d_in[16];
+    p.gbr   = (const float*)d_in[17];
+    p.gatt  = (const float*)d_in[18];
+    p.gbias = (const float*)d_in[19];
+    p.n2w   = (const float*)d_in[20];
+    p.n2b   = (const float*)d_in[21];
+    p.n2ms  = (const float*)d_in[22];
+    p.v1w   = (const float*)d_in[23];
+    p.v1b   = (const float*)d_in[24];
+    p.v2w   = (const float*)d_in[25];
+    p.v2b   = (const float*)d_in[26];
+    p.v3w   = (const float*)d_in[27];
+    p.v3b   = (const float*)d_in[28];
+    p.a1w   = (const float*)d_in[29];
+    p.a1b   = (const float*)d_in[30];
+    p.a2w   = (const float*)d_in[31];
+    p.a2b   = (const float*)d_in[32];
+    p.a3w   = (const float*)d_in[33];
+    p.a3b   = (const float*)d_in[34];
+    p.out   = (float*)d_out;
 
     uint8_t* wsb = (uint8_t*)d_ws;
-    uint32_t* fwdb = (uint32_t*)wsb;
-    uint32_t* trsb = (uint32_t*)(wsb + 524288);
-    uint32_t* Rb   = (uint32_t*)(wsb + 1048576);
-    unsigned short* csrF = (unsigned short*)(wsb + 1572864);
-    unsigned short* csrT = csrF + (size_t)MAXD * 8192;
-    float* h_raw  = (float*)(csrT + (size_t)MAXD * 8192);
-    float* x1     = h_raw + (size_t)NNt * 3;
-    float* colsum = x1 + (size_t)NNt * 3;
-    float* g_raw  = colsum + NNt;
-    float* xpg    = g_raw + (size_t)BB * KPAD * 3;
-    float4* xlg   = (float4*)(xpg + (size_t)BB * KPAD * 3);
-    int*   kidxg  = (int*)(xlg + (size_t)BB * KP2);
-    uint32_t* RTg = (uint32_t*)(kidxg + (size_t)BB * KPAD);
-    const size_t needed = 1572864
-                        + 2 * (size_t)MAXD * 8192 * 2
-                        + ((size_t)(2 * NNt * 3 + NNt
-                           + 2 * BB * KPAD * 3)) * 4
-                        + (size_t)BB * KP2 * 16
-                        + (size_t)BB * KPAD * 4
-                        + (size_t)BB * 16 * KP2 * 4;
+    p.fwdb = (uint32_t*)wsb;
+    p.trsb = (uint32_t*)(wsb + 524288);
+    p.bar  = (uint32_t*)(wsb + 1048576);
+    p.Rb   = (uint32_t*)(wsb + 1048832);
+    p.csrF = (unsigned short*)(wsb + 1048832 + 524288);
+    p.csrT = p.csrF + (size_t)MAXD * 8192;
+    p.h_raw  = (float*)(p.csrT + (size_t)MAXD * 8192);
+    p.x1     = p.h_raw + (size_t)NNt * 3;
+    p.colsum = p.x1 + (size_t)NNt * 3;
+    p.g_raw  = p.colsum + NNt;
+    p.xpg    = p.g_raw + (size_t)BB * KPAD * 3;
+    p.xlg    = (float4*)(p.xpg + (size_t)BB * KPAD * 3);
+    p.kidxg  = (int*)(p.xlg + (size_t)BB * KP2);
+    p.RTg    = (uint32_t*)(p.kidxg + (size_t)BB * KPAD);
+    const size_t needed = (size_t)((uint8_t*)(p.RTg + (size_t)BB * 16 * KP2) - wsb);
     if (ws_size < needed) return;
 
-    hipMemsetAsync(fwdb, 0, 1048576, stream);
-    r17_scatter<<<dim3((EEe + 255) / 256), dim3(256), 0, stream>>>(ei, fwdb, trsb);
-    r17_extract<<<dim3(64), dim3(256), 0, stream>>>(fwdb, trsb, csrF, csrT);
-    r19_mid<<<dim3(16, 12), dim3(512), 0, stream>>>(x, csrF, csrT, panw, l1w, l1b,
-                                                    h_raw, colsum, Rb);
-    r19_pool<<<dim3(16), dim3(512), 0, stream>>>(h_raw, colsum, Rb,
-                                                 n1w, n1b, n1ms, poolp, poolb,
-                                                 gwl, gbl,
-                                                 x1, xpg, xlg, kidxg, RTg);
-    r19_gat<<<dim3(16, 52), dim3(512), 0, stream>>>(xpg, xlg, kidxg, RTg,
-                                                    gwr, gbr, gatt, gbias, g_raw);
-    r17_head<<<dim3(16), dim3(512), 0, stream>>>(g_raw, x1, x, cnid, amask,
-                                                 n2w, n2b, n2ms, v1w, v1b, v2w, v2b, v3w, v3b,
-                                                 a1w, a1b, a2w, a2b, a3w, a3b, out);
+    hipMemsetAsync(p.bar, 0, 256, stream);
+    r20_mega<<<dim3(NBLK), dim3(512), 0, stream>>>(p);
 }
```

Result: slower. 350.2 us (+73.7%).
